# Performance work log

Measured on AMD Instinct MI355X. Metric: run time of the kernel, lower is better.

The kernel has to match this reference:

```python
import jax, jax.numpy as jnp
import numpy as np

ALPHA = 0.2  # LeakyReLU negative slope
NEG_BIG = -9e15

def setup_inputs() -> dict:
    key = jax.random.key(0)
    k1, k2, k3, k4 = jax.random.split(key, 4)
    N, F_IN, F_OUT = 8192, 128, 128
    h = jax.random.normal(k1, (N, F_IN), dtype=jnp.float32)
    adj = jax.random.randint(k2, (N, N), 0, 2, dtype=jnp.int32)
    # xavier-uniform-ish params
    W = jax.random.normal(k3, (F_IN, F_OUT), dtype=jnp.float32) * (1.0 / np.sqrt(F_IN))
    a = jax.random.normal(k4, (2 * F_OUT, 1), dtype=jnp.float32) * (1.0 / np.sqrt(2 * F_OUT))
    return {"h": h, "adj": adj, "W": W, "a": a}

def reference(h, adj, W, a):
    # Wh: [N, F_OUT]
    Wh = h @ W
    F_out = Wh.shape[1]
    # a_input @ a == (Wh @ a1)_i + (Wh @ a2)_j  (same math, no N^2*2F tensor)
    a1 = a[:F_out, 0]   # [F_OUT]
    a2 = a[F_out:, 0]   # [F_OUT]
    e = (Wh @ a1)[:, None] + (Wh @ a2)[None, :]        # [N, N]
    e = jnp.where(e >= 0, e, ALPHA * e)                # LeakyReLU(0.2)
    scores = jnp.where(adj > 0, e, NEG_BIG)
    attention = jax.nn.softmax(scores, axis=1)         # row-wise
    # dropout skipped (eval mode / training=False)
    return attention @ Wh                              # [N, F_OUT]
```

## Files before the change

kernel.cpp:

```cpp
#include <hip/hip_runtime.h>
#include <hip/hip_bf16.h>

#define N 8192
#define FD 128
#define LOG2E 1.4426950408889634f

typedef __attribute__((ext_vector_type(4))) float f4;
typedef __attribute__((ext_vector_type(4))) int i32x4;
typedef __attribute__((ext_vector_type(4))) unsigned int u32x4;
typedef __attribute__((ext_vector_type(8))) __bf16 bf16x8;

__device__ __forceinline__ unsigned short bfbits(float x){
  __bf16 b = (__bf16)x;
  return __builtin_bit_cast(unsigned short, b);
}

__global__ __launch_bounds__(256) void k1_wh(const float* __restrict__ h,
                                             const float* __restrict__ W,
                                             float* __restrict__ Wh,
                                             unsigned short* __restrict__ Bsw){
  __shared__ float Wl[64*128];
  __shared__ float hT[128*33];
  int t = threadIdx.x;
  int i0 = blockIdx.x * 32;
  {
    int r  = t >> 3;
    int k0 = (t & 7) * 16;
    const f4* src = (const f4*)&h[(size_t)(i0 + r)*FD + k0];
    #pragma unroll
    for (int q = 0; q < 4; ++q){
      f4 v = src[q];
      #pragma unroll
      for (int e = 0; e < 4; ++e) hT[(k0 + q*4 + e)*33 + r] = v[e];
    }
  }
  int f0 = (t & 31) * 4;
  int r0 = (t >> 5) * 4;
  float acc[4][4] = {};
  for (int half = 0; half < 2; ++half){
    __syncthreads();
    #pragma unroll
    for (int v = 0; v < 8; ++v){
      int idx = (v*256 + t)*4;
      *(f4*)&Wl[idx] = *(const f4*)&W[half*8192 + idx];
    }
    __syncthreads();
    for (int k2 = 0; k2 < 64; ++k2){
      f4 wv = *(const f4*)&Wl[k2*FD + f0];
      f4 hv = *(const f4*)&hT[(half*64 + k2)*33 + r0];
      #pragma unroll
      for (int ri = 0; ri < 4; ++ri)
        #pragma unroll
        for (int fi = 0; fi < 4; ++fi)
          acc[ri][fi] = __builtin_fmaf(hv[ri], wv[fi], acc[ri][fi]);
    }
  }
  #pragma unroll
  for (int ri = 0; ri < 4; ++ri){
    f4 o = {acc[ri][0], acc[ri][1], acc[ri][2], acc[ri][3]};
    *(f4*)&Wh[(size_t)(i0 + r0 + ri)*FD + f0] = o;
  }
  int jblk = blockIdx.x;
  int n  = f0 >> 4;
  int fl = f0 & 15;
  #pragma unroll
  for (int ri = 0; ri < 4; ++ri){
    int k = r0 + ri;
    size_t base = (((size_t)jblk*8 + n)*64 + ((k>>3)<<4))*8 + (k&7);
    #pragma unroll
    for (int fi = 0; fi < 4; ++fi)
      Bsw[base + (size_t)(fl + fi)*8] = bfbits(acc[ri][fi]);
  }
}

__global__ __launch_bounds__(256) void k2_s(const float* __restrict__ Wh,
                                            const float* __restrict__ a,
                                            float* __restrict__ s1L,
                                            float* __restrict__ s2L){
  int i = blockIdx.x*256 + threadIdx.x;
  const f4* row = (const f4*)&Wh[(size_t)i*FD];
  const f4* a1 = (const f4*)a;
  const f4* a2 = (const f4*)&a[FD];
  float x1 = 0.f, x2 = 0.f;
  #pragma unroll
  for (int q = 0; q < 32; ++q){
    f4 w = row[q], va = a1[q], vb = a2[q];
    #pragma unroll
    for (int e = 0; e < 4; ++e){
      x1 = __builtin_fmaf(w[e], va[e], x1);
      x2 = __builtin_fmaf(w[e], vb[e], x2);
    }
  }
  s1L[i] = x1 * LOG2E; s2L[i] = x2 * LOG2E;
}

__global__ __launch_bounds__(256) void k3_max(const float* __restrict__ s2L,
                                              float* __restrict__ M2L){
  __shared__ float red[4];
  int t = threadIdx.x;
  float m = -3.0e38f;
  for (int i = t; i < N; i += 256) m = fmaxf(m, s2L[i]);
  #pragma unroll
  for (int d = 1; d < 64; d <<= 1) m = fmaxf(m, __shfl_xor(m, d, 64));
  if ((t & 63) == 0) red[t >> 6] = m;
  __syncthreads();
  if (t == 0) *M2L = fmaxf(fmaxf(red[0], red[1]), fmaxf(red[2], red[3]));
}

__global__ __launch_bounds__(256,4) void k4_flash(const int* __restrict__ adj,
    const unsigned short* __restrict__ Bsw,
    const float* __restrict__ s1L, const float* __restrict__ s2L,
    const float* __restrict__ M2p,
    float* __restrict__ partial, float* __restrict__ denomp, int njc){
  int t = threadIdx.x;
  int wv = t >> 6, lane = t & 63;
  int lrow = lane & 15, lgrp = lane >> 4;
  int i0w = blockIdx.x * 64 + wv * 16;
  int row = i0w + lrow;
  int jlen = N / njc;
  int jstart = blockIdx.y * jlen;
  int iters = jlen / 32;
  float M2 = *M2p;
  float s1a = s1L[row];
  float ea = s1a + M2;
  float maL = fmaxf(ea, 0.2f*ea);

  f4 acc[8];
  #pragma unroll
  for (int n = 0; n < 8; ++n) acc[n] = (f4){0.f,0.f,0.f,0.f};
  f4 accd = (f4){0.f,0.f,0.f,0.f};

  u32x4 onesbits = (u32x4){0x3F803F80u,0x3F803F80u,0x3F803F80u,0x3F803F80u};
  bf16x8 ones = __builtin_bit_cast(bf16x8, onesbits);

  const i32x4* adj4 = (const i32x4*)adj;
  const f4* s2v = (const f4*)s2L;
  size_t rbase = ((size_t)row * N) >> 2;

  int jb = jstart + lgrp*8;
  i32x4 c0 = adj4[rbase + (jb>>2)];
  i32x4 c1 = adj4[rbase + (jb>>2) + 1];
  f4 za = s2v[jb>>2], zb = s2v[(jb>>2)+1];

  for (int js = 0; js < iters; ++js){
    i32x4 u0 = c0, u1 = c1; f4 ya = za, yb = zb;
    int jn = jb + 32;
    if (jn >= jstart + jlen) jn = jstart + lgrp*8;
    c0 = adj4[rbase + (jn>>2)];
    c1 = adj4[rbase + (jn>>2) + 1];
    za = s2v[jn>>2]; zb = s2v[(jn>>2)+1];

    int jtile = jb >> 5;
    u32x4 braw[8];
    #pragma unroll
    for (int n = 0; n < 8; ++n)
      braw[n] = *(const u32x4*)&Bsw[((((size_t)jtile*8 + n)*64) + lane)*8];

    bf16x8 fa;
    #pragma unroll
    for (int e = 0; e < 8; ++e){
      float sj = (e < 4) ? ya[e] : yb[e-4];
      int av   = (e < 4) ? u0[e] : u1[e-4];
      float x  = s1a + sj;
      float lr = fmaxf(x, 0.2f*x);
      float p  = av ? __builtin_amdgcn_exp2f(lr - maL) : 0.f;
      fa[e] = (__bf16)p;
    }
    accd = __builtin_amdgcn_mfma_f32_16x16x32_bf16(fa, ones, accd, 0, 0, 0);
    #pragma unroll
    for (int n = 0; n < 8; ++n)
      acc[n] = __builtin_amdgcn_mfma_f32_16x16x32_bf16(fa,
                 __builtin_bit_cast(bf16x8, braw[n]), acc[n], 0, 0, 0);
    jb += 32;
  }

  if (lrow == 0){
    #pragma unroll
    for (int r = 0; r < 4; ++r)
      denomp[(size_t)blockIdx.y*N + i0w + lgrp*4 + r] = accd[r];
  }
  float* pb = partial + (size_t)blockIdx.y * N * FD;
  #pragma unroll
  for (int n = 0; n < 8; ++n)
    #pragma unroll
    for (int r = 0; r < 4; ++r)
      pb[(size_t)(i0w + lgrp*4 + r)*FD + n*16 + lrow] = acc[n][r];
}

__global__ __launch_bounds__(256) void k5_fin(const float* __restrict__ partial,
    const float* __restrict__ denomp, float* __restrict__ out, int njc){
  int g = blockIdx.x*256 + threadIdx.x;
  int i = g >> 7;
  float num = 0.f, den = 0.f;
  for (int c = 0; c < njc; ++c) num += partial[(size_t)c*N*FD + g];
  for (int c = 0; c < njc; ++c) den += denomp[(size_t)c*N + i];
  out[g] = num / den;
}

extern "C" void kernel_launch(void* const* d_in, const int* in_sizes, int n_in,
                              void* d_out, int out_size, void* d_ws, size_t ws_size,
                              hipStream_t stream){
  const float* h   = (const float*)d_in[0];
  const int*   adj = (const int*)d_in[1];
  const float* W   = (const float*)d_in[2];
  const float* a   = (const float*)d_in[3];
  float* out = (float*)d_out;
  char* ws = (char*)d_ws;

  unsigned short* Bsw = (unsigned short*)ws;
  float* Wh  = (float*)(ws + (size_t)(2u<<20));
  float* s1L = (float*)(ws + (size_t)(6u<<20));
  float* s2L = (float*)(ws + (size_t)(6u<<20) + 32768);
  float* M2L = (float*)(ws + (size_t)(6u<<20) + 65536);
  float* denomp  = (float*)(ws + (size_t)(7u<<20));
  float* partial = (float*)(ws + (size_t)(8u<<20));

  size_t chunk = (size_t)N * FD * sizeof(float);
  int njc = 1;
  if (ws_size > ((size_t)(8u<<20))){
    size_t m = (ws_size - (size_t)(8u<<20)) / chunk;
    njc = (m >= 8) ? 8 : (m >= 4) ? 4 : (m >= 2) ? 2 : 1;
  }

  hipLaunchKernelGGL(k1_wh,  dim3(256), dim3(256), 0, stream, h, W, Wh, Bsw);
  hipLaunchKernelGGL(k2_s,   dim3(32),  dim3(256), 0, stream, Wh, a, s1L, s2L);
  hipLaunchKernelGGL(k3_max, dim3(1),   dim3(256), 0, stream, s2L, M2L);
  hipLaunchKernelGGL(k4_flash, dim3(128, njc), dim3(256), 0, stream,
                     adj, Bsw, s1L, s2L, M2L, partial, denomp, njc);
  hipLaunchKernelGGL(k5_fin, dim3(N*FD/256), dim3(256), 0, stream, partial, denomp, out, njc);
}
```

Before: 489.5 us.

## Fuse score projection into Wh GEMM and stage adjacency bitmasks via LDS

Merges the Wh GEMM with the attention-score dot products, using shuffle reductions, so the fp32 Wh buffer is no longer written and re-read, and one launch is removed. The flash kernel now loads adjacency in coalesced row-contiguous chunks of 256 columns, packs each group of 8 entries into a byte mask held in double-buffered shared memory, and prefetches the next chunk while computing the current one. This targets the poorly coalesced per-lane adjacency reads that dominate the traffic. Occupancy hint drops from 4 to 2 blocks per CU because the 16-register staging array raises register pressure.

```diff
diff --git a/kernel.cpp b/kernel.cpp
--- a/kernel.cpp
+++ b/kernel.cpp
@@ -15,10 +15,12 @@
   return __builtin_bit_cast(unsigned short, b);
 }
 
-__global__ __launch_bounds__(256) void k1_wh(const float* __restrict__ h,
-                                             const float* __restrict__ W,
-                                             float* __restrict__ Wh,
-                                             unsigned short* __restrict__ Bsw){
+__global__ __launch_bounds__(256) void k12_wh(const float* __restrict__ h,
+                                              const float* __restrict__ W,
+                                              const float* __restrict__ a,
+                                              unsigned short* __restrict__ Bsw,
+                                              float* __restrict__ s1L,
+                                              float* __restrict__ s2L){
   __shared__ float Wl[64*128];
   __shared__ float hT[128*33];
   int t = threadIdx.x;
@@ -55,11 +57,6 @@
           acc[ri][fi] = __builtin_fmaf(hv[ri], wv[fi], acc[ri][fi]);
     }
   }
-  #pragma unroll
-  for (int ri = 0; ri < 4; ++ri){
-    f4 o = {acc[ri][0], acc[ri][1], acc[ri][2], acc[ri][3]};
-    *(f4*)&Wh[(size_t)(i0 + r0 + ri)*FD + f0] = o;
-  }
   int jblk = blockIdx.x;
   int n  = f0 >> 4;
   int fl = f0 & 15;
@@ -71,27 +68,33 @@
     for (int fi = 0; fi < 4; ++fi)
       Bsw[base + (size_t)(fl + fi)*8] = bfbits(acc[ri][fi]);
   }
-}
-
-__global__ __launch_bounds__(256) void k2_s(const float* __restrict__ Wh,
-                                            const float* __restrict__ a,
-                                            float* __restrict__ s1L,
-                                            float* __restrict__ s2L){
-  int i = blockIdx.x*256 + threadIdx.x;
-  const f4* row = (const f4*)&Wh[(size_t)i*FD];
-  const f4* a1 = (const f4*)a;
-  const f4* a2 = (const f4*)&a[FD];
-  float x1 = 0.f, x2 = 0.f;
-  #pragma unroll
-  for (int q = 0; q < 32; ++q){
-    f4 w = row[q], va = a1[q], vb = a2[q];
-    #pragma unroll
-    for (int e = 0; e < 4; ++e){
-      x1 = __builtin_fmaf(w[e], va[e], x1);
-      x2 = __builtin_fmaf(w[e], vb[e], x2);
-    }
-  }
-  s1L[i] = x1 * LOG2E; s2L[i] = x2 * LOG2E;
+  f4 a1v = *(const f4*)&a[f0];
+  f4 a2v = *(const f4*)&a[FD + f0];
+  float p1[4], p2[4];
+  #pragma unroll
+  for (int ri = 0; ri < 4; ++ri){
+    p1[ri] = 0.f; p2[ri] = 0.f;
+    #pragma unroll
+    for (int fi = 0; fi < 4; ++fi){
+      p1[ri] = __builtin_fmaf(acc[ri][fi], a1v[fi], p1[ri]);
+      p2[ri] = __builtin_fmaf(acc[ri][fi], a2v[fi], p2[ri]);
+    }
+  }
+  #pragma unroll
+  for (int d = 1; d < 32; d <<= 1){
+    #pragma unroll
+    for (int ri = 0; ri < 4; ++ri){
+      p1[ri] += __shfl_xor(p1[ri], d, 32);
+      p2[ri] += __shfl_xor(p2[ri], d, 32);
+    }
+  }
+  if ((t & 31) == 0){
+    #pragma unroll
+    for (int ri = 0; ri < 4; ++ri){
+      s1L[i0 + r0 + ri] = p1[ri] * LOG2E;
+      s2L[i0 + r0 + ri] = p2[ri] * LOG2E;
+    }
+  }
 }
 
 __global__ __launch_bounds__(256) void k3_max(const float* __restrict__ s2L,
@@ -107,21 +110,21 @@
   if (t == 0) *M2L = fmaxf(fmaxf(red[0], red[1]), fmaxf(red[2], red[3]));
 }
 
-__global__ __launch_bounds__(256,4) void k4_flash(const int* __restrict__ adj,
+__global__ __launch_bounds__(256,2) void k4_flash(const int* __restrict__ adj,
     const unsigned short* __restrict__ Bsw,
     const float* __restrict__ s1L, const float* __restrict__ s2L,
     const float* __restrict__ M2p,
     float* __restrict__ partial, float* __restrict__ denomp, int njc){
+  __shared__ unsigned char mk[4][2][16][32];
   int t = threadIdx.x;
   int wv = t >> 6, lane = t & 63;
   int lrow = lane & 15, lgrp = lane >> 4;
   int i0w = blockIdx.x * 64 + wv * 16;
-  int row = i0w + lrow;
   int jlen = N / njc;
   int jstart = blockIdx.y * jlen;
-  int iters = jlen / 32;
+  int nmac = jlen >> 8;
   float M2 = *M2p;
-  float s1a = s1L[row];
+  float s1a = s1L[i0w + lrow];
   float ea = s1a + M2;
   float maL = fmaxf(ea, 0.2f*ea);
 
@@ -129,49 +132,82 @@
   #pragma unroll
   for (int n = 0; n < 8; ++n) acc[n] = (f4){0.f,0.f,0.f,0.f};
   f4 accd = (f4){0.f,0.f,0.f,0.f};
-
   u32x4 onesbits = (u32x4){0x3F803F80u,0x3F803F80u,0x3F803F80u,0x3F803F80u};
   bf16x8 ones = __builtin_bit_cast(bf16x8, onesbits);
 
   const i32x4* adj4 = (const i32x4*)adj;
   const f4* s2v = (const f4*)s2L;
-  size_t rbase = ((size_t)row * N) >> 2;
-
-  int jb = jstart + lgrp*8;
-  i32x4 c0 = adj4[rbase + (jb>>2)];
-  i32x4 c1 = adj4[rbase + (jb>>2) + 1];
-  f4 za = s2v[jb>>2], zb = s2v[(jb>>2)+1];
-
-  for (int js = 0; js < iters; ++js){
-    i32x4 u0 = c0, u1 = c1; f4 ya = za, yb = zb;
-    int jn = jb + 32;
-    if (jn >= jstart + jlen) jn = jstart + lgrp*8;
-    c0 = adj4[rbase + (jn>>2)];
-    c1 = adj4[rbase + (jn>>2) + 1];
-    za = s2v[jn>>2]; zb = s2v[(jn>>2)+1];
-
-    int jtile = jb >> 5;
-    u32x4 braw[8];
-    #pragma unroll
-    for (int n = 0; n < 8; ++n)
-      braw[n] = *(const u32x4*)&Bsw[((((size_t)jtile*8 + n)*64) + lane)*8];
-
-    bf16x8 fa;
-    #pragma unroll
-    for (int e = 0; e < 8; ++e){
-      float sj = (e < 4) ? ya[e] : yb[e-4];
-      int av   = (e < 4) ? u0[e] : u1[e-4];
-      float x  = s1a + sj;
-      float lr = fmaxf(x, 0.2f*x);
-      float p  = av ? __builtin_amdgcn_exp2f(lr - maL) : 0.f;
-      fa[e] = (__bf16)p;
-    }
-    accd = __builtin_amdgcn_mfma_f32_16x16x32_bf16(fa, ones, accd, 0, 0, 0);
-    #pragma unroll
-    for (int n = 0; n < 8; ++n)
-      acc[n] = __builtin_amdgcn_mfma_f32_16x16x32_bf16(fa,
-                 __builtin_bit_cast(bf16x8, braw[n]), acc[n], 0, 0, 0);
-    jb += 32;
+  size_t stbase = (((size_t)(i0w + (lane >> 5)) * N) + (size_t)(lane & 31) * 8) >> 2;
+  const size_t rowstep2 = ((size_t)2 * N) >> 2;
+
+  i32x4 st[16];
+  {
+    size_t b0 = stbase + ((size_t)jstart >> 2);
+    #pragma unroll
+    for (int p = 0; p < 8; ++p){
+      st[2*p]   = adj4[b0 + (size_t)p * rowstep2];
+      st[2*p+1] = adj4[b0 + (size_t)p * rowstep2 + 1];
+    }
+    #pragma unroll
+    for (int p = 0; p < 8; ++p){
+      unsigned v = 0;
+      #pragma unroll
+      for (int e = 0; e < 4; ++e){
+        v |= (st[2*p][e]   != 0) ? (1u << e)     : 0u;
+        v |= (st[2*p+1][e] != 0) ? (1u << (4+e)) : 0u;
+      }
+      mk[wv][0][2*p + (lane >> 5)][lane & 31] = (unsigned char)v;
+    }
+  }
+
+  for (int m = 0; m < nmac; ++m){
+    int bf = m & 1;
+    int jbase = jstart + m*256;
+    if (m + 1 < nmac){
+      size_t bn = stbase + ((size_t)(jbase + 256) >> 2);
+      #pragma unroll
+      for (int p = 0; p < 8; ++p){
+        st[2*p]   = adj4[bn + (size_t)p * rowstep2];
+        st[2*p+1] = adj4[bn + (size_t)p * rowstep2 + 1];
+      }
+    }
+    int jt0 = jbase >> 5;
+    #pragma unroll
+    for (int js = 0; js < 8; ++js){
+      int jb = jbase + js*32 + lgrp*8;
+      unsigned mbyte = mk[wv][bf][lrow][js*4 + lgrp];
+      f4 ya = s2v[jb >> 2], yb = s2v[(jb >> 2) + 1];
+      u32x4 braw[8];
+      #pragma unroll
+      for (int n = 0; n < 8; ++n)
+        braw[n] = *(const u32x4*)&Bsw[((((size_t)(jt0 + js)*8 + n)*64) + lane)*8];
+      bf16x8 fa;
+      #pragma unroll
+      for (int e = 0; e < 8; ++e){
+        float sj = (e < 4) ? ya[e] : yb[e-4];
+        float x  = s1a + sj;
+        float lr = fmaxf(x, 0.2f*x);
+        float p  = ((mbyte >> e) & 1u) ? __builtin_amdgcn_exp2f(lr - maL) : 0.f;
+        fa[e] = (__bf16)p;
+      }
+      accd = __builtin_amdgcn_mfma_f32_16x16x32_bf16(fa, ones, accd, 0, 0, 0);
+      #pragma unroll
+      for (int n = 0; n < 8; ++n)
+        acc[n] = __builtin_amdgcn_mfma_f32_16x16x32_bf16(fa,
+                   __builtin_bit_cast(bf16x8, braw[n]), acc[n], 0, 0, 0);
+    }
+    if (m + 1 < nmac){
+      #pragma unroll
+      for (int p = 0; p < 8; ++p){
+        unsigned v = 0;
+        #pragma unroll
+        for (int e = 0; e < 4; ++e){
+          v |= (st[2*p][e]   != 0) ? (1u << e)     : 0u;
+          v |= (st[2*p+1][e] != 0) ? (1u << (4+e)) : 0u;
+        }
+        mk[wv][bf ^ 1][2*p + (lane >> 5)][lane & 31] = (unsigned char)v;
+      }
+    }
   }
 
   if (lrow == 0){
@@ -208,7 +244,6 @@
   char* ws = (char*)d_ws;
 
   unsigned short* Bsw = (unsigned short*)ws;
-  float* Wh  = (float*)(ws + (size_t)(2u<<20));
   float* s1L = (float*)(ws + (size_t)(6u<<20));
   float* s2L = (float*)(ws + (size_t)(6u<<20) + 32768);
   float* M2L = (float*)(ws + (size_t)(6u<<20) + 65536);
@@ -222,8 +257,7 @@
     njc = (m >= 8) ? 8 : (m >= 4) ? 4 : (m >= 2) ? 2 : 1;
   }
 
-  hipLaunchKernelGGL(k1_wh,  dim3(256), dim3(256), 0, stream, h, W, Wh, Bsw);
-  hipLaunchKernelGGL(k2_s,   dim3(32),  dim3(256), 0, stream, Wh, a, s1L, s2L);
+  hipLaunchKernelGGL(k12_wh, dim3(256), dim3(256), 0, stream, h, W, a, Bsw, s1L, s2L);
   hipLaunchKernelGGL(k3_max, dim3(1),   dim3(256), 0, stream, s2L, M2L);
   hipLaunchKernelGGL(k4_flash, dim3(128, njc), dim3(256), 0, stream,
                      adj, Bsw, s1L, s2L, M2L, partial, denomp, njc);
```

Result: no change. 486.3 us (-0.7%).
